# Performance work log

Hardware: AMD Instinct MI355X
Metric: run time of the kernel (lower is better)

Reference implementation:

```python
import jax, jax.numpy as jnp
import numpy as np

N_USERS = 100000
N_ITEMS = 50000
N_NODES = N_USERS + N_ITEMS
NNZ = 4000000
BATCH = 16384
DIM = 64
ALPHA = 0.1
K_LAYERS = 3


def setup_inputs() -> dict:
    key = jax.random.key(0)
    ks = jax.random.split(key, 7)
    user_emb = 0.1 * jax.random.normal(ks[0], (N_USERS, DIM), dtype=jnp.float32)
    item_emb = 0.1 * jax.random.normal(ks[1], (N_ITEMS, DIM), dtype=jnp.float32)
    edge_vals = jax.random.uniform(ks[2], (NNZ,), dtype=jnp.float32)
    row = jax.random.randint(ks[3], (NNZ,), 0, N_NODES, dtype=jnp.int32)
    col = jax.random.randint(ks[4], (NNZ,), 0, N_NODES, dtype=jnp.int32)
    users = jax.random.randint(ks[5], (BATCH,), 0, N_USERS, dtype=jnp.int32)
    items = jax.random.randint(ks[6], (BATCH,), 0, N_ITEMS, dtype=jnp.int32)
    return {"user_emb": user_emb, "item_emb": item_emb, "edge_vals": edge_vals,
            "row": row, "col": col, "users": users, "items": items}


def _propagate(user_emb, item_emb, edge_vals, row, col):
    # computer(): concat user/item embeddings, then APPNP/PPR-style propagation
    # x^{k+1} = alpha * x0 + (1-alpha) * A x^k   (A sparse COO, symmetric-normalized)
    x0 = jnp.concatenate([user_emb, item_emb], axis=0)  # [N, d]
    x = x0
    w = edge_vals[:, None]
    for _ in range(K_LAYERS):
        msg = w * x[col]  # gather: [nnz, d]
        agg = jax.ops.segment_sum(msg, row, num_segments=N_NODES)  # scatter-add spmm
        x = ALPHA * x0 + (1.0 - ALPHA) * agg
    return x[:N_USERS], x[N_USERS:]


def reference(user_emb, item_emb, edge_vals, row, col, users, items):
    all_users, all_items = _propagate(user_emb, item_emb, edge_vals, row, col)
    u = all_users[users]   # [B, d]
    i = all_items[items]   # [B, d]
    gamma = jnp.sum(u * i, axis=1)  # [B]
    return gamma
```

## Files before the change

kernel.cpp:

```cpp
#include <hip/hip_runtime.h>

#define N_USERS 100000
#define N_ITEMS 50000
#define N_NODES 150000
#define NNZ_EDGES 4000000
#define BATCH_SZ 16384
#define DIM 64
#define ALPHA 0.1f
#define BETA 0.9f

#define BKT_SHIFT 9
#define BKT_ROWS  (1 << BKT_SHIFT)
#define NBKT      ((N_NODES + BKT_ROWS - 1) >> BKT_SHIFT)
#define BKT_CAP   16384
#define BKT_PAD   16
#define BIN_CHUNK 4096
#define N_BIN_BLOCKS ((NNZ_EDGES + BIN_CHUNK - 1) / BIN_CHUNK)

__device__ __forceinline__ unsigned short gtn_f2bf(float f) {
    unsigned int u = __float_as_uint(f);
    u = u + 0x7FFFu + ((u >> 16) & 1u);
    return (unsigned short)(u >> 16);
}

__global__ void gtn_cvt_kernel(const float* __restrict__ xu,
                               const float* __restrict__ xi,
                               unsigned short* __restrict__ x0b) {
    const int total4 = N_NODES * DIM / 4;
    const int boundary4 = N_USERS * DIM / 4;
    for (int i4 = blockIdx.x * blockDim.x + threadIdx.x; i4 < total4;
         i4 += gridDim.x * blockDim.x) {
        const float4 v = (i4 < boundary4)
            ? ((const float4*)xu)[i4]
            : ((const float4*)xi)[i4 - boundary4];
        ushort4 o;
        o.x = gtn_f2bf(v.x);
        o.y = gtn_f2bf(v.y);
        o.z = gtn_f2bf(v.z);
        o.w = gtn_f2bf(v.w);
        ((ushort4*)x0b)[i4] = o;
    }
}

__global__ void gtn_bin_scatter_kernel(const int* __restrict__ row,
                                       const int* __restrict__ col,
                                       const float* __restrict__ w,
                                       int* __restrict__ bucketCnt,
                                       int2* __restrict__ binned) {
    __shared__ int lcnt[NBKT];
    __shared__ int lbase[NBKT];
    const int chunkStart = blockIdx.x * BIN_CHUNK;
    const int chunkEnd = min(chunkStart + BIN_CHUNK, NNZ_EDGES);

    for (int b = threadIdx.x; b < NBKT; b += blockDim.x) lcnt[b] = 0;
    __syncthreads();
    for (int e = chunkStart + threadIdx.x; e < chunkEnd; e += blockDim.x)
        atomicAdd(&lcnt[row[e] >> BKT_SHIFT], 1);
    __syncthreads();
    for (int b = threadIdx.x; b < NBKT; b += blockDim.x) {
        const int c = lcnt[b];
        lbase[b] = c ? atomicAdd(&bucketCnt[b * BKT_PAD], c) : 0;
        lcnt[b] = 0;
    }
    __syncthreads();
    for (int e = chunkStart + threadIdx.x; e < chunkEnd; e += blockDim.x) {
        const int r = row[e];
        const int b = r >> BKT_SHIFT;
        const int lr = atomicAdd(&lcnt[b], 1);
        const int pos = b * BKT_CAP + lbase[b] + lr;
        binned[pos] = make_int2(col[e] | ((r & (BKT_ROWS - 1)) << 18),
                                __float_as_int(w[e]));
    }
}

__global__ void gtn_bktbase_kernel(const int* __restrict__ bucketCnt,
                                   int* __restrict__ bktBase) {
    __shared__ int s[512];
    const int t = threadIdx.x;
    const int v = (t < NBKT) ? bucketCnt[t * BKT_PAD] : 0;
    s[t] = v;
    __syncthreads();
    for (int off = 1; off < 512; off <<= 1) {
        const int tv = (t >= off) ? s[t - off] : 0;
        __syncthreads();
        s[t] += tv;
        __syncthreads();
    }
    if (t < NBKT) bktBase[t] = s[t] - v;
}

__global__ void gtn_bucket_csr_kernel(const int2* __restrict__ binned,
                                      const int* __restrict__ bucketCnt,
                                      const int* __restrict__ bktBase,
                                      int* __restrict__ rowPtr,
                                      int* __restrict__ cnt,
                                      int2* __restrict__ colw) {
    __shared__ int hist[BKT_ROWS];
    __shared__ int scan[BKT_ROWS];
    __shared__ int cursor[BKT_ROWS];
    const int b = blockIdx.x;
    const int t = threadIdx.x;
    hist[t] = 0;
    __syncthreads();
    const int n = bucketCnt[b * BKT_PAD];
    const int2* src = binned + (size_t)b * BKT_CAP;
    for (int e = t; e < n; e += BKT_ROWS)
        atomicAdd(&hist[((unsigned)src[e].x) >> 18], 1);
    __syncthreads();
    const int v = hist[t];
    scan[t] = v;
    __syncthreads();
    for (int off = 1; off < BKT_ROWS; off <<= 1) {
        const int tv = (t >= off) ? scan[t - off] : 0;
        __syncthreads();
        scan[t] += tv;
        __syncthreads();
    }
    const int g = (b << BKT_SHIFT) + t;
    const int pos0 = bktBase[b] + scan[t] - v;
    if (g < N_NODES) { cnt[g] = v; rowPtr[g] = pos0; }
    cursor[t] = pos0;
    __syncthreads();
    for (int e = t; e < n; e += BKT_ROWS) {
        const int2 ed = src[e];
        const int inrow = ((unsigned)ed.x) >> 18;
        const int pos = atomicAdd(&cursor[inrow], 1);
        colw[pos] = make_int2(ed.x & 0x3FFFF, ed.y);
    }
}

__device__ __forceinline__ float4 gtn_gather_row_bf16(
        int node, int lane, int sub, int grp,
        const unsigned short* __restrict__ x,
        const int* __restrict__ rowPtr, const int* __restrict__ cnt,
        const int2* __restrict__ colw) {
    const int start = rowPtr[node];
    const int n = cnt[node];
    float4 acc = make_float4(0.f, 0.f, 0.f, 0.f);
    for (int base = 0; base < n; base += 64) {
        const int m = min(64, n - base);
        int2 e = make_int2(0, 0);
        if (lane < m) e = colw[start + base + lane];
        const int nj = (m + 3) >> 2;
        for (int jb = 0; jb < nj; jb += 4) {
            uint2 xv[4];
            float wv[4];
#pragma unroll
            for (int k = 0; k < 4; ++k) {
                const int src = ((jb + k) << 2) + grp;
                const int c = __shfl(e.x, src, 64);
                wv[k] = __int_as_float(__shfl(e.y, src, 64));
                xv[k] = *(const uint2*)(x + ((size_t)c << 6) + (sub << 2));
            }
#pragma unroll
            for (int k = 0; k < 4; ++k) {
                acc.x = fmaf(wv[k], __uint_as_float(xv[k].x << 16), acc.x);
                acc.y = fmaf(wv[k], __uint_as_float(xv[k].x & 0xFFFF0000u), acc.y);
                acc.z = fmaf(wv[k], __uint_as_float(xv[k].y << 16), acc.z);
                acc.w = fmaf(wv[k], __uint_as_float(xv[k].y & 0xFFFF0000u), acc.w);
            }
        }
    }
    return acc;
}

__device__ __forceinline__ float4 gtn_reduce_groups(float4 a) {
    a.x += __shfl_xor(a.x, 16, 64);
    a.y += __shfl_xor(a.y, 16, 64);
    a.z += __shfl_xor(a.z, 16, 64);
    a.w += __shfl_xor(a.w, 16, 64);
    a.x += __shfl_xor(a.x, 32, 64);
    a.y += __shfl_xor(a.y, 32, 64);
    a.z += __shfl_xor(a.z, 32, 64);
    a.w += __shfl_xor(a.w, 32, 64);
    return a;
}

__device__ __forceinline__ void gtn_store_bf16_row(unsigned short* out,
                                                   int node, int sub, float4 o) {
    ushort4 o4;
    o4.x = gtn_f2bf(o.x);
    o4.y = gtn_f2bf(o.y);
    o4.z = gtn_f2bf(o.z);
    o4.w = gtn_f2bf(o.w);
    ((ushort4*)(out + (size_t)node * DIM))[sub] = o4;
}

__global__ void gtn_layer_kernel(const unsigned short* __restrict__ x,
                                 const float* __restrict__ x0u,
                                 const float* __restrict__ x0i,
                                 const int* __restrict__ rowPtr,
                                 const int* __restrict__ cnt,
                                 const int2* __restrict__ colw,
                                 unsigned short* __restrict__ out) {
    const int lane = threadIdx.x & 63;
    const int sub = lane & 15;
    const int grp = lane >> 4;
    const int node = (blockIdx.x * blockDim.x + threadIdx.x) >> 6;
    if (node >= N_NODES) return;
    float4 agg = gtn_gather_row_bf16(node, lane, sub, grp, x, rowPtr, cnt, colw);
    agg = gtn_reduce_groups(agg);
    if (grp == 0) {
        const float4 x0v = (node < N_USERS)
            ? ((const float4*)(x0u + (size_t)node * DIM))[sub]
            : ((const float4*)(x0i + (size_t)(node - N_USERS) * DIM))[sub];
        float4 o;
        o.x = ALPHA * x0v.x + BETA * agg.x;
        o.y = ALPHA * x0v.y + BETA * agg.y;
        o.z = ALPHA * x0v.z + BETA * agg.z;
        o.w = ALPHA * x0v.w + BETA * agg.w;
        gtn_store_bf16_row(out, node, sub, o);
    }
}

__global__ void gtn_l3_dot_kernel(const unsigned short* __restrict__ x,
                                  const float* __restrict__ x0u,
                                  const float* __restrict__ x0i,
                                  const int* __restrict__ rowPtr,
                                  const int* __restrict__ cnt,
                                  const int2* __restrict__ colw,
                                  const int* __restrict__ users,
                                  const int* __restrict__ items,
                                  float* __restrict__ out) {
    const int lane = threadIdx.x & 63;
    const int sub = lane & 15;
    const int grp = lane >> 4;
    const int b = (blockIdx.x * blockDim.x + threadIdx.x) >> 6;
    if (b >= BATCH_SZ) return;
    const int u = users[b];
    const int it = items[b] + N_USERS;

    float4 au = gtn_gather_row_bf16(u, lane, sub, grp, x, rowPtr, cnt, colw);
    au = gtn_reduce_groups(au);
    float4 ai = gtn_gather_row_bf16(it, lane, sub, grp, x, rowPtr, cnt, colw);
    ai = gtn_reduce_groups(ai);

    const float4 x0uv = ((const float4*)(x0u + (size_t)u * DIM))[sub];
    const float4 x0iv = ((const float4*)(x0i + (size_t)(it - N_USERS) * DIM))[sub];
    float4 vu, vi;
    vu.x = ALPHA * x0uv.x + BETA * au.x;  vi.x = ALPHA * x0iv.x + BETA * ai.x;
    vu.y = ALPHA * x0uv.y + BETA * au.y;  vi.y = ALPHA * x0iv.y + BETA * ai.y;
    vu.z = ALPHA * x0uv.z + BETA * au.z;  vi.z = ALPHA * x0iv.z + BETA * ai.z;
    vu.w = ALPHA * x0uv.w + BETA * au.w;  vi.w = ALPHA * x0iv.w + BETA * ai.w;

    float p = vu.x * vi.x + vu.y * vi.y + vu.z * vi.z + vu.w * vi.w;
    p += __shfl_xor(p, 1, 64);
    p += __shfl_xor(p, 2, 64);
    p += __shfl_xor(p, 4, 64);
    p += __shfl_xor(p, 8, 64);
    if (lane == 0) out[b] = p;
}

extern "C" void kernel_launch(void* const* d_in, const int* in_sizes, int n_in,
                              void* d_out, int out_size, void* d_ws, size_t ws_size,
                              hipStream_t stream) {
    const float* user_emb  = (const float*)d_in[0];
    const float* item_emb  = (const float*)d_in[1];
    const float* edge_vals = (const float*)d_in[2];
    const int*   row       = (const int*)d_in[3];
    const int*   col       = (const int*)d_in[4];
    const int*   users     = (const int*)d_in[5];
    const int*   items     = (const int*)d_in[6];
    float* out = (float*)d_out;

    char* p = (char*)d_ws;
    unsigned short* x0b  = (unsigned short*)p; p += (size_t)N_NODES * DIM * 2;
    unsigned short* bufA = (unsigned short*)p; p += (size_t)N_NODES * DIM * 2;
    unsigned short* bufB = (unsigned short*)p; p += (size_t)N_NODES * DIM * 2;
    int2*  colw      = (int2*)p; p += (size_t)NNZ_EDGES * sizeof(int2);
    int2*  binned    = (int2*)p; p += (size_t)NBKT * BKT_CAP * sizeof(int2);
    int*   bucketCnt = (int*)p;  p += (size_t)NBKT * BKT_PAD * sizeof(int);
    int*   bktBase   = (int*)p;  p += 512 * sizeof(int);
    int*   cnt       = (int*)p;  p += (size_t)N_NODES * sizeof(int);
    int*   rowPtr    = (int*)p;  p += (size_t)N_NODES * sizeof(int);

    const dim3 blk(256);

    hipMemsetAsync(bucketCnt, 0, (size_t)NBKT * BKT_PAD * sizeof(int), stream);
    gtn_bin_scatter_kernel<<<dim3(N_BIN_BLOCKS), dim3(512), 0, stream>>>(
        row, col, edge_vals, bucketCnt, binned);
    gtn_cvt_kernel<<<dim3(2048), blk, 0, stream>>>(user_emb, item_emb, x0b);
    gtn_bktbase_kernel<<<dim3(1), dim3(512), 0, stream>>>(bucketCnt, bktBase);
    gtn_bucket_csr_kernel<<<dim3(NBKT), dim3(BKT_ROWS), 0, stream>>>(
        binned, bucketCnt, bktBase, rowPtr, cnt, colw);

    const dim3 layerGrid((N_NODES * 64 + 255) / 256);
    gtn_layer_kernel<<<layerGrid, blk, 0, stream>>>(
        x0b, user_emb, item_emb, rowPtr, cnt, colw, bufA);
    gtn_layer_kernel<<<layerGrid, blk, 0, stream>>>(
        bufA, user_emb, item_emb, rowPtr, cnt, colw, bufB);
    const dim3 dotGrid((BATCH_SZ * 64) / 256);
    gtn_l3_dot_kernel<<<dotGrid, blk, 0, stream>>>(
        bufB, user_emb, item_emb, rowPtr, cnt, colw, users, items, out);
}
```

Baseline: 297.4 us.

## Sort edges per chunk in shared memory before writing binned output

The binning kernel now counting-sorts each 4096-edge chunk by bucket in shared memory and writes it contiguously, recording per-(bucket, chunk) segment offsets. This replaces scattered global writes into fixed-capacity bucket regions and drops the BKT_CAP overflow assumption. The CSR build kernel now uses 1024 threads, each walking one chunk's segment serially. Those serial loops have uneven lengths and read sequentially per thread, so the gather phase may lose coalescing in exchange for coalesced writes in the binning step.

New measurement: 328.6 us. +10.5%, slower.

```diff
diff --git a/kernel.cpp b/kernel.cpp
--- a/kernel.cpp
+++ b/kernel.cpp
@@ -12,7 +12,6 @@
 #define BKT_SHIFT 9
 #define BKT_ROWS  (1 << BKT_SHIFT)
 #define NBKT      ((N_NODES + BKT_ROWS - 1) >> BKT_SHIFT)
-#define BKT_CAP   16384
 #define BKT_PAD   16
 #define BIN_CHUNK 4096
 #define N_BIN_BLOCKS ((NNZ_EDGES + BIN_CHUNK - 1) / BIN_CHUNK)
@@ -42,42 +41,80 @@
     }
 }
 
-__global__ void gtn_bin_scatter_kernel(const int* __restrict__ row,
-                                       const int* __restrict__ col,
-                                       const float* __restrict__ w,
-                                       int* __restrict__ bucketCnt,
-                                       int2* __restrict__ binned) {
-    __shared__ int lcnt[NBKT];
-    __shared__ int lbase[NBKT];
-    const int chunkStart = blockIdx.x * BIN_CHUNK;
-    const int chunkEnd = min(chunkStart + BIN_CHUNK, NNZ_EDGES);
-
-    for (int b = threadIdx.x; b < NBKT; b += blockDim.x) lcnt[b] = 0;
-    __syncthreads();
-    for (int e = chunkStart + threadIdx.x; e < chunkEnd; e += blockDim.x)
-        atomicAdd(&lcnt[row[e] >> BKT_SHIFT], 1);
-    __syncthreads();
-    for (int b = threadIdx.x; b < NBKT; b += blockDim.x) {
-        const int c = lcnt[b];
-        lbase[b] = c ? atomicAdd(&bucketCnt[b * BKT_PAD], c) : 0;
-        lcnt[b] = 0;
-    }
-    __syncthreads();
-    for (int e = chunkStart + threadIdx.x; e < chunkEnd; e += blockDim.x) {
-        const int r = row[e];
-        const int b = r >> BKT_SHIFT;
-        const int lr = atomicAdd(&lcnt[b], 1);
-        const int pos = b * BKT_CAP + lbase[b] + lr;
-        binned[pos] = make_int2(col[e] | ((r & (BKT_ROWS - 1)) << 18),
-                                __float_as_int(w[e]));
-    }
-}
-
-__global__ void gtn_bktbase_kernel(const int* __restrict__ bucketCnt,
+__global__ void gtn_bin_sort_kernel(const int* __restrict__ row,
+                                    const int* __restrict__ col,
+                                    const float* __restrict__ w,
+                                    int2* __restrict__ binned,
+                                    int2* __restrict__ blkSeg,
+                                    int* __restrict__ bucketTotal) {
+    __shared__ int hist[NBKT];
+    __shared__ int scanb[512];
+    __shared__ int cursor[NBKT];
+    __shared__ int2 stage[BIN_CHUNK];
+    const int blk = blockIdx.x;
+    const int t = threadIdx.x;
+    const int chunkStart = blk * BIN_CHUNK;
+    const int chunkN = min(BIN_CHUNK, NNZ_EDGES - chunkStart);
+
+    for (int b = t; b < NBKT; b += 512) hist[b] = 0;
+    __syncthreads();
+
+    int rloc[BIN_CHUNK / 512];
+#pragma unroll
+    for (int k = 0; k < BIN_CHUNK / 512; ++k) {
+        const int i = t + k * 512;
+        int r = -1;
+        if (i < chunkN) {
+            r = row[chunkStart + i];
+            atomicAdd(&hist[r >> BKT_SHIFT], 1);
+        }
+        rloc[k] = r;
+    }
+    __syncthreads();
+
+    const int hv = (t < NBKT) ? hist[t] : 0;
+    scanb[t] = hv;
+    __syncthreads();
+    for (int off = 1; off < 512; off <<= 1) {
+        const int tv = (t >= off) ? scanb[t - off] : 0;
+        __syncthreads();
+        scanb[t] += tv;
+        __syncthreads();
+    }
+    if (t < NBKT) {
+        const int exc = scanb[t] - hv;
+        cursor[t] = exc;
+        blkSeg[(size_t)t * N_BIN_BLOCKS + blk] = make_int2(exc, hv);
+        if (hv) atomicAdd(&bucketTotal[t * BKT_PAD], hv);
+    }
+    __syncthreads();
+
+#pragma unroll
+    for (int k = 0; k < BIN_CHUNK / 512; ++k) {
+        const int i = t + k * 512;
+        if (i < chunkN) {
+            const int r = rloc[k];
+            const int b = r >> BKT_SHIFT;
+            const int pos = atomicAdd(&cursor[b], 1);
+            stage[pos] = make_int2(col[chunkStart + i] | ((r & (BKT_ROWS - 1)) << 18),
+                                   __float_as_int(w[chunkStart + i]));
+        }
+    }
+    __syncthreads();
+
+    int2* dst = binned + (size_t)chunkStart;
+#pragma unroll
+    for (int k = 0; k < BIN_CHUNK / 512; ++k) {
+        const int i = t + k * 512;
+        if (i < chunkN) dst[i] = stage[i];
+    }
+}
+
+__global__ void gtn_bktbase_kernel(const int* __restrict__ bucketTotal,
                                    int* __restrict__ bktBase) {
     __shared__ int s[512];
     const int t = threadIdx.x;
-    const int v = (t < NBKT) ? bucketCnt[t * BKT_PAD] : 0;
+    const int v = (t < NBKT) ? bucketTotal[t * BKT_PAD] : 0;
     s[t] = v;
     __syncthreads();
     for (int off = 1; off < 512; off <<= 1) {
@@ -90,7 +127,7 @@
 }
 
 __global__ void gtn_bucket_csr_kernel(const int2* __restrict__ binned,
-                                      const int* __restrict__ bucketCnt,
+                                      const int2* __restrict__ blkSeg,
                                       const int* __restrict__ bktBase,
                                       int* __restrict__ rowPtr,
                                       int* __restrict__ cnt,
@@ -100,29 +137,39 @@
     __shared__ int cursor[BKT_ROWS];
     const int b = blockIdx.x;
     const int t = threadIdx.x;
-    hist[t] = 0;
-    __syncthreads();
-    const int n = bucketCnt[b * BKT_PAD];
-    const int2* src = binned + (size_t)b * BKT_CAP;
-    for (int e = t; e < n; e += BKT_ROWS)
-        atomicAdd(&hist[((unsigned)src[e].x) >> 18], 1);
-    __syncthreads();
-    const int v = hist[t];
-    scan[t] = v;
+    if (t < BKT_ROWS) hist[t] = 0;
+    __syncthreads();
+
+    int2 seg = make_int2(0, 0);
+    const int2* p0 = binned;
+    if (t < N_BIN_BLOCKS) {
+        seg = blkSeg[(size_t)b * N_BIN_BLOCKS + t];
+        p0 = binned + (size_t)t * BIN_CHUNK + seg.x;
+    }
+    for (int j = 0; j < seg.y; ++j)
+        atomicAdd(&hist[((unsigned)p0[j].x) >> 18], 1);
+    __syncthreads();
+
+    const int v = (t < BKT_ROWS) ? hist[t] : 0;
+    if (t < BKT_ROWS) scan[t] = v;
     __syncthreads();
     for (int off = 1; off < BKT_ROWS; off <<= 1) {
-        const int tv = (t >= off) ? scan[t - off] : 0;
-        __syncthreads();
-        scan[t] += tv;
-        __syncthreads();
-    }
-    const int g = (b << BKT_SHIFT) + t;
-    const int pos0 = bktBase[b] + scan[t] - v;
-    if (g < N_NODES) { cnt[g] = v; rowPtr[g] = pos0; }
-    cursor[t] = pos0;
-    __syncthreads();
-    for (int e = t; e < n; e += BKT_ROWS) {
-        const int2 ed = src[e];
+        int tv = 0;
+        if (t < BKT_ROWS && t >= off) tv = scan[t - off];
+        __syncthreads();
+        if (t < BKT_ROWS) scan[t] += tv;
+        __syncthreads();
+    }
+    if (t < BKT_ROWS) {
+        const int g = (b << BKT_SHIFT) + t;
+        const int pos0 = bktBase[b] + scan[t] - v;
+        if (g < N_NODES) { cnt[g] = v; rowPtr[g] = pos0; }
+        cursor[t] = pos0;
+    }
+    __syncthreads();
+
+    for (int j = 0; j < seg.y; ++j) {
+        const int2 ed = p0[j];
         const int inrow = ((unsigned)ed.x) >> 18;
         const int pos = atomicAdd(&cursor[inrow], 1);
         colw[pos] = make_int2(ed.x & 0x3FFFF, ed.y);
@@ -267,22 +314,23 @@
     unsigned short* x0b  = (unsigned short*)p; p += (size_t)N_NODES * DIM * 2;
     unsigned short* bufA = (unsigned short*)p; p += (size_t)N_NODES * DIM * 2;
     unsigned short* bufB = (unsigned short*)p; p += (size_t)N_NODES * DIM * 2;
-    int2*  colw      = (int2*)p; p += (size_t)NNZ_EDGES * sizeof(int2);
-    int2*  binned    = (int2*)p; p += (size_t)NBKT * BKT_CAP * sizeof(int2);
-    int*   bucketCnt = (int*)p;  p += (size_t)NBKT * BKT_PAD * sizeof(int);
-    int*   bktBase   = (int*)p;  p += 512 * sizeof(int);
-    int*   cnt       = (int*)p;  p += (size_t)N_NODES * sizeof(int);
-    int*   rowPtr    = (int*)p;  p += (size_t)N_NODES * sizeof(int);
+    int2*  colw        = (int2*)p; p += (size_t)NNZ_EDGES * sizeof(int2);
+    int2*  binned      = (int2*)p; p += (size_t)NNZ_EDGES * sizeof(int2);
+    int2*  blkSeg      = (int2*)p; p += (size_t)NBKT * N_BIN_BLOCKS * sizeof(int2);
+    int*   bucketTotal = (int*)p;  p += (size_t)NBKT * BKT_PAD * sizeof(int);
+    int*   bktBase     = (int*)p;  p += 512 * sizeof(int);
+    int*   cnt         = (int*)p;  p += (size_t)N_NODES * sizeof(int);
+    int*   rowPtr      = (int*)p;  p += (size_t)N_NODES * sizeof(int);
 
     const dim3 blk(256);
 
-    hipMemsetAsync(bucketCnt, 0, (size_t)NBKT * BKT_PAD * sizeof(int), stream);
-    gtn_bin_scatter_kernel<<<dim3(N_BIN_BLOCKS), dim3(512), 0, stream>>>(
-        row, col, edge_vals, bucketCnt, binned);
+    hipMemsetAsync(bucketTotal, 0, (size_t)NBKT * BKT_PAD * sizeof(int), stream);
+    gtn_bin_sort_kernel<<<dim3(N_BIN_BLOCKS), dim3(512), 0, stream>>>(
+        row, col, edge_vals, binned, blkSeg, bucketTotal);
     gtn_cvt_kernel<<<dim3(2048), blk, 0, stream>>>(user_emb, item_emb, x0b);
-    gtn_bktbase_kernel<<<dim3(1), dim3(512), 0, stream>>>(bucketCnt, bktBase);
-    gtn_bucket_csr_kernel<<<dim3(NBKT), dim3(BKT_ROWS), 0, stream>>>(
-        binned, bucketCnt, bktBase, rowPtr, cnt, colw);
+    gtn_bktbase_kernel<<<dim3(1), dim3(512), 0, stream>>>(bucketTotal, bktBase);
+    gtn_bucket_csr_kernel<<<dim3(NBKT), dim3(1024), 0, stream>>>(
+        binned, blkSeg, bktBase, rowPtr, cnt, colw);
 
     const dim3 layerGrid((N_NODES * 64 + 255) / 256);
     gtn_layer_kernel<<<layerGrid, blk, 0, stream>>>(
```
